# Performance work log

Measured on AMD Instinct MI355X. Metric: run time of the kernel, lower is better.

## Reference

```python
import jax, jax.numpy as jnp
import numpy as np
from jax import lax

H = 145; W = 145; BANDS = 200; D_MODEL = 128; NUM_CLASSES = 17
# Mamba2 defaults: expand=2, headdim=64, d_state=128, d_conv=4, ngroups=1
D_INNER = 256; NHEADS = 4; HEADDIM = 64; D_STATE = 128; D_CONV = 4
D_IN_PROJ = 2 * D_INNER + 2 * D_STATE + NHEADS  # 772
CONV_DIM = D_INNER + 2 * D_STATE                # 512


def _gelu(x):
    return jax.nn.gelu(x, approximate=False)


def _ln(x, g, b, eps=1e-5):
    m = jnp.mean(x, -1, keepdims=True)
    v = jnp.mean((x - m) ** 2, -1, keepdims=True)
    return (x - m) * lax.rsqrt(v + eps) * g + b


def _adaptive_pool_last(x, out):
    # PyTorch AdaptiveAvgPool semantics along the last axis via integral image
    L = x.shape[-1]
    i = np.arange(out)
    starts = (i * L) // out
    ends = -((-(i + 1) * L) // out)  # ceil((i+1)*L/out)
    cs = jnp.concatenate([jnp.zeros(x.shape[:-1] + (1,), x.dtype), jnp.cumsum(x, -1)], -1)
    return (cs[..., ends] - cs[..., starts]) / jnp.asarray(ends - starts, x.dtype)


def _mamba2(u, in_w, conv_w, conv_b, dt_bias, A_log, D, norm_w, out_w):
    # u: (L, D_MODEL). Faithful Mamba2 reference path (batch=1 squeezed).
    L = u.shape[0]
    zxbcdt = u @ in_w                      # (L, 772)
    z = zxbcdt[:, :D_INNER]                # (L, 256)
    xBC = zxbcdt[:, D_INNER:2 * D_INNER + 2 * D_STATE]  # (L, 512)
    dt = jax.nn.softplus(zxbcdt[:, -NHEADS:] + dt_bias)  # (L, 4)
    # causal depthwise conv1d, kernel D_CONV, then SiLU
    xp = jnp.pad(xBC, ((D_CONV - 1, 0), (0, 0)))
    xBC = sum(xp[k:k + L] * conv_w[:, k] for k in range(D_CONV)) + conv_b
    xBC = jax.nn.silu(xBC)
    xh = xBC[:, :D_INNER].reshape(L, NHEADS, HEADDIM)     # (L, h, p)
    Bm = xBC[:, D_INNER:D_INNER + D_STATE]                # (L, n)
    Cm = xBC[:, D_INNER + D_STATE:]                       # (L, n)
    A = -jnp.exp(A_log)                                   # (h,)

    def step(state, inp):
        dt_t, x_t, B_t, C_t = inp          # (h,), (h,p), (n,), (n,)
        dA = jnp.exp(dt_t * A)             # (h,)
        state = state * dA[:, None, None] + (dt_t[:, None] * x_t)[:, :, None] * B_t[None, None, :]
        y_t = jnp.einsum('hpn,n->hp', state, C_t)
        return state, y_t

    s0 = jnp.zeros((NHEADS, HEADDIM, D_STATE), u.dtype)
    _, y = lax.scan(step, s0, (dt, xh, Bm, Cm))           # y: (L, h, p)
    y = y + D[None, :, None] * xh
    y = y.reshape(L, D_INNER) * jax.nn.silu(z)            # gated
    y = y * lax.rsqrt(jnp.mean(y * y, -1, keepdims=True) + 1e-5) * norm_w  # RMSNormGated
    return y @ out_w                                      # (L, D_MODEL)


def _forward(x, ln_pre_g, ln_pre_b, fe_w1, fe_b1, fe_w2, fe_b2,
             cv_w1, cv_b1, cv_w2, cv_b2, mp_w, mp_b, mp_ln_g, mp_ln_b,
             m_in_w, m_conv_w, m_conv_b, m_dt_bias, m_A_log, m_D, m_norm_w, m_out_w,
             cls_ln_g, cls_ln_b, cls_w1, cls_b1, cls_w2, cls_b2, cls_w3, cls_b3):
    h, w, _ = x.shape
    xn = _ln(x, ln_pre_g, ln_pre_b)
    # MLP feature branch
    f = _gelu(xn @ fe_w1 + fe_b1)
    f = _gelu(f @ fe_w2 + fe_b2)                          # (h, w, 128)
    # conv branch
    c = jnp.transpose(xn, (2, 0, 1))[None]                # (1, bands, h, w)
    dn = ('NCHW', 'OIHW', 'NCHW')
    c = lax.conv_general_dilated(c, cv_w1, (1, 1), [(2, 2), (2, 2)], dimension_numbers=dn)
    c = _gelu(c + cv_b1[None, :, None, None])             # (1, 32, 147, 147)
    c = lax.conv_general_dilated(c, cv_w2, (1, 1), [(1, 1), (1, 1)], dimension_numbers=dn)
    c = _gelu(c + cv_b2[None, :, None, None])             # (1, 64, 147, 147)
    c = _adaptive_pool_last(c, W)                         # pool width -> 145
    c = _adaptive_pool_last(c.swapaxes(-1, -2), H).swapaxes(-1, -2)  # pool height
    conv_feat = jnp.transpose(c[0], (1, 2, 0))            # (145, 145, 64)
    comb = jnp.concatenate([f, conv_feat], -1).reshape(h * w, 192)
    p = _gelu(_ln(comb @ mp_w + mp_b, mp_ln_g, mp_ln_b))  # (L, d_model)
    m = _mamba2(p, m_in_w, m_conv_w, m_conv_b, m_dt_bias, m_A_log, m_D, m_norm_w, m_out_w)
    r = m.reshape(h, w, D_MODEL)
    o = _ln(r, cls_ln_g, cls_ln_b)
    o = _gelu(o @ cls_w1 + cls_b1)
    o = _gelu(o @ cls_w2 + cls_b2)
    return o @ cls_w3 + cls_b3                            # (h, w, num_classes)


def setup_inputs() -> dict:
    key = jax.random.key(0)
    ks = jax.random.split(key, 16)
    def n(k, shape, s=0.02):
        return jax.random.normal(k, shape, jnp.float32) * s
    return dict(
        x=jax.random.normal(ks[0], (H, W, BANDS), jnp.float32),
        ln_pre_g=jnp.ones((BANDS,), jnp.float32), ln_pre_b=jnp.zeros((BANDS,), jnp.float32),
        fe_w1=n(ks[1], (BANDS, 256)), fe_b1=jnp.zeros((256,), jnp.float32),
        fe_w2=n(ks[2], (256, 128)), fe_b2=jnp.zeros((128,), jnp.float32),
        cv_w1=n(ks[3], (32, BANDS, 3, 3)), cv_b1=jnp.zeros((32,), jnp.float32),
        cv_w2=n(ks[4], (64, 32, 3, 3)), cv_b2=jnp.zeros((64,), jnp.float32),
        mp_w=n(ks[5], (192, D_MODEL)), mp_b=jnp.zeros((D_MODEL,), jnp.float32),
        mp_ln_g=jnp.ones((D_MODEL,), jnp.float32), mp_ln_b=jnp.zeros((D_MODEL,), jnp.float32),
        m_in_w=n(ks[6], (D_MODEL, D_IN_PROJ)),
        m_conv_w=n(ks[7], (CONV_DIM, D_CONV), 0.2), m_conv_b=jnp.zeros((CONV_DIM,), jnp.float32),
        m_dt_bias=jnp.full((NHEADS,), -4.0, jnp.float32),
        m_A_log=jnp.log(jnp.linspace(1.0, 16.0, NHEADS)).astype(jnp.float32),
        m_D=jnp.ones((NHEADS,), jnp.float32),
        m_norm_w=jnp.ones((D_INNER,), jnp.float32),
        m_out_w=n(ks[8], (D_INNER, D_MODEL)),
        cls_ln_g=jnp.ones((D_MODEL,), jnp.float32), cls_ln_b=jnp.zeros((D_MODEL,), jnp.float32),
        cls_w1=n(ks[9], (D_MODEL, 128)), cls_b1=jnp.zeros((128,), jnp.float32),
        cls_w2=n(ks[10], (128, 64)), cls_b2=jnp.zeros((64,), jnp.float32),
        cls_w3=n(ks[11], (64, NUM_CLASSES)), cls_b3=jnp.zeros((NUM_CLASSES,), jnp.float32),
    )


def reference(x, ln_pre_g, ln_pre_b, fe_w1, fe_b1, fe_w2, fe_b2,
              cv_w1, cv_b1, cv_w2, cv_b2, mp_w, mp_b, mp_ln_g, mp_ln_b,
              m_in_w, m_conv_w, m_conv_b, m_dt_bias, m_A_log, m_D, m_norm_w, m_out_w,
              cls_ln_g, cls_ln_b, cls_w1, cls_b1, cls_w2, cls_b2, cls_w3, cls_b3):
    return _forward(x, ln_pre_g, ln_pre_b, fe_w1, fe_b1, fe_w2, fe_b2,
                    cv_w1, cv_b1, cv_w2, cv_b2, mp_w, mp_b, mp_ln_g, mp_ln_b,
                    m_in_w, m_conv_w, m_conv_b, m_dt_bias, m_A_log, m_D, m_norm_w, m_out_w,
                    cls_ln_g, cls_ln_b, cls_w1, cls_b1, cls_w2, cls_b2, cls_w3, cls_b3)
```

## Files before the change

kernel.cpp:

```cpp
#include <hip/hip_runtime.h>
#include <math.h>

#define HW 21025
#define Hdim 145
#define Wdim 145
#define NBANDS 200
#define CONVH 147
#define CONVHW 21609
#define QC 64
#define NCH 329
#define DTP 21056
#define SP 72

typedef __attribute__((ext_vector_type(4))) float fv4;
typedef __attribute__((ext_vector_type(8))) short short8;

#define OFF_XN   ((size_t)0)
#define OFF_F1   ((size_t)4205000)
#define OFF_COMB ((size_t)9587400)
#define OFF_P    ((size_t)13624200)
#define OFF_ZX   ((size_t)16315400)
#define OFF_XBC  ((size_t)32546700)
#define OFF_S    ((size_t)43311500)
#define OFF_DT   ((size_t)54092172)
#define OFF_CT   ((size_t)54176396)
#define OFF_W    ((size_t)54177712)

__device__ __forceinline__ float gelu_f(float x){
    return 0.5f * x * (1.0f + erff(x * 0.70710678118654752440f));
}
__device__ __forceinline__ float silu_f(float x){
    return x / (1.0f + expf(-x));
}

__device__ __forceinline__ void bf16_split(float x, unsigned short& hs, unsigned short& ls){
    unsigned u = __float_as_uint(x);
    hs = (unsigned short)(u >> 16);
    float hif = __uint_as_float(u & 0xFFFF0000u);
    float lof = x - hif;
    ls = (unsigned short)(__float_as_uint(lof) >> 16);
}
__device__ __forceinline__ unsigned pack2(unsigned short a, unsigned short b){
    return (unsigned)a | ((unsigned)b << 16);
}

template<int ACT>
__global__ void ln_kernel(const float* __restrict__ in, const float* __restrict__ g,
                          const float* __restrict__ b, float* __restrict__ out, int D){
    int row = blockIdx.x, tid = threadIdx.x;
    const float* r = in + (size_t)row * D;
    float s = 0.f, s2 = 0.f;
    for (int i = tid; i < D; i += 256){ float v = r[i]; s += v; s2 += v*v; }
    __shared__ float r1[4], r2[4];
    #pragma unroll
    for (int o = 32; o > 0; o >>= 1){ s += __shfl_down(s, o); s2 += __shfl_down(s2, o); }
    if ((tid & 63) == 0){ r1[tid >> 6] = s; r2[tid >> 6] = s2; }
    __syncthreads();
    float S = r1[0] + r1[1] + r1[2] + r1[3];
    float S2 = r2[0] + r2[1] + r2[2] + r2[3];
    float mean = S / (float)D;
    float var = S2 / (float)D - mean * mean;
    float rs = rsqrtf(fmaxf(var, 0.f) + 1e-5f);
    float* o_ = out + (size_t)row * D;
    for (int i = tid; i < D; i += 256){
        float v = (r[i] - mean) * rs * g[i] + b[i];
        if (ACT == 1) v = gelu_f(v);
        o_[i] = v;
    }
}

template<int ACT>
__global__ __launch_bounds__(256) void gemm_mfma(const float* __restrict__ A, int lda,
                                                 const float* __restrict__ B,
                                                 const float* __restrict__ bias,
                                                 float* __restrict__ C, int ldc,
                                                 int M, int N, int K){
    const int SA = 40;
    __shared__ __align__(16) unsigned short Ah[128 * SA], Al[128 * SA];
    __shared__ __align__(16) unsigned short Bh[64 * SA],  Bl[64 * SA];
    int tid = threadIdx.x;
    int lane = tid & 63, wid = tid >> 6;
    int wy = wid >> 1, wx = wid & 1;
    int bm = blockIdx.y * 128, bn = blockIdx.x * 64;
    int l15 = lane & 15, g = lane >> 4;

    fv4 acc[4][2];
    #pragma unroll
    for (int i = 0; i < 4; i++)
        #pragma unroll
        for (int j = 0; j < 2; j++) acc[i][j] = (fv4){0.f,0.f,0.f,0.f};

    int am = tid >> 1;
    int aq = (tid & 1) * 4;
    bool arow_ok = (bm + am) < M;
    int bn_t = tid & 63;
    int bk8 = (tid >> 6) * 8;
    bool bcol_ok = (bn + bn_t) < N;

    int nK = (K + 31) / 32;
    for (int ks = 0; ks < nK; ks++){
        int k0 = ks * 32;
        const float* Ap = A + (size_t)(bm + am) * lda + k0;
        #pragma unroll
        for (int f = 0; f < 4; f++){
            int kq = aq + f;
            fv4 v = (fv4){0.f,0.f,0.f,0.f};
            if (arow_ok && (k0 + kq * 4 + 4) <= K)
                v = *reinterpret_cast<const fv4*>(Ap + kq * 4);
            unsigned short hs[4], ls[4];
            #pragma unroll
            for (int j = 0; j < 4; j++) bf16_split(v[j], hs[j], ls[j]);
            unsigned off = am * SA + kq * 4;
            *reinterpret_cast<uint2*>(&Ah[off]) = make_uint2(pack2(hs[0],hs[1]), pack2(hs[2],hs[3]));
            *reinterpret_cast<uint2*>(&Al[off]) = make_uint2(pack2(ls[0],ls[1]), pack2(ls[2],ls[3]));
        }
        {
            unsigned short hs[8], ls[8];
            #pragma unroll
            for (int j = 0; j < 8; j++){
                int kk = k0 + bk8 + j;
                float v = (bcol_ok && kk < K) ? B[(size_t)kk * N + bn + bn_t] : 0.f;
                bf16_split(v, hs[j], ls[j]);
            }
            unsigned off = bn_t * SA + bk8;
            *reinterpret_cast<uint4*>(&Bh[off]) = make_uint4(pack2(hs[0],hs[1]), pack2(hs[2],hs[3]),
                                                             pack2(hs[4],hs[5]), pack2(hs[6],hs[7]));
            *reinterpret_cast<uint4*>(&Bl[off]) = make_uint4(pack2(ls[0],ls[1]), pack2(ls[2],ls[3]),
                                                             pack2(ls[4],ls[5]), pack2(ls[6],ls[7]));
        }
        __syncthreads();
        short8 afh[4], afl[4], bfh[2], bfl[2];
        #pragma unroll
        for (int mi = 0; mi < 4; mi++){
            unsigned off = (wy * 64 + mi * 16 + l15) * SA + g * 8;
            afh[mi] = *reinterpret_cast<const short8*>(&Ah[off]);
            afl[mi] = *reinterpret_cast<const short8*>(&Al[off]);
        }
        #pragma unroll
        for (int ni = 0; ni < 2; ni++){
            unsigned off = (wx * 32 + ni * 16 + l15) * SA + g * 8;
            bfh[ni] = *reinterpret_cast<const short8*>(&Bh[off]);
            bfl[ni] = *reinterpret_cast<const short8*>(&Bl[off]);
        }
        #pragma unroll
        for (int mi = 0; mi < 4; mi++)
            #pragma unroll
            for (int ni = 0; ni < 2; ni++){
                acc[mi][ni] = __builtin_amdgcn_mfma_f32_16x16x32_bf16(afh[mi], bfh[ni], acc[mi][ni], 0, 0, 0);
                acc[mi][ni] = __builtin_amdgcn_mfma_f32_16x16x32_bf16(afh[mi], bfl[ni], acc[mi][ni], 0, 0, 0);
                acc[mi][ni] = __builtin_amdgcn_mfma_f32_16x16x32_bf16(afl[mi], bfh[ni], acc[mi][ni], 0, 0, 0);
            }
        __syncthreads();
    }
    #pragma unroll
    for (int mi = 0; mi < 4; mi++){
        #pragma unroll
        for (int ni = 0; ni < 2; ni++){
            int cc = bn + wx * 32 + ni * 16 + l15;
            if (cc >= N) continue;
            float bv = bias ? bias[cc] : 0.f;
            #pragma unroll
            for (int j = 0; j < 4; j++){
                int rr = bm + wy * 64 + mi * 16 + g * 4 + j;
                if (rr >= M) continue;
                float v = acc[mi][ni][j] + bv;
                if (ACT == 1) v = gelu_f(v);
                C[(size_t)rr * ldc + cc] = v;
            }
        }
    }
}

template<int IC, int OC, int NCHUNK>
__global__ void prep_w(const float* __restrict__ w, unsigned short* __restrict__ Wh,
                       unsigned short* __restrict__ Wl){
    const int KP = NCHUNK * 288;
    int idx = blockIdx.x * 256 + threadIdx.x;
    if (idx >= OC * KP) return;
    int o = idx / KP, k = idx % KP;
    int ch = k / 288, rest = k % 288, t = rest / 32, c = rest & 31;
    int ci = ch * 32 + c;
    float v = (ci < IC) ? w[((size_t)o * IC + ci) * 9 + t] : 0.f;
    unsigned short hs, ls;
    bf16_split(v, hs, ls);
    Wh[idx] = hs; Wl[idx] = ls;
}

template<int IC, int OC, int PAD, int NCHUNK, int NFRAG>
__global__ __launch_bounds__(256) void conv_mfma(const float* __restrict__ in,
                                                 int inH, int inW,
                                                 const unsigned short* __restrict__ Wh,
                                                 const unsigned short* __restrict__ Wl,
                                                 const float* __restrict__ bias,
                                                 float* __restrict__ out){
    const int KP = NCHUNK * 288;
    const int CST = 40;
    __shared__ __align__(16) unsigned short Xh[3 * 68 * CST], Xl[3 * 68 * CST];
    int y = blockIdx.y;
    int x0 = blockIdx.x * 64;
    int tid = threadIdx.x;
    int lane = tid & 63, wid = tid >> 6;
    int wy = wid >> 1, wx = wid & 1;
    int l15 = lane & 15, g = lane >> 4;

    fv4 acc[2][NFRAG];
    #pragma unroll
    for (int mi = 0; mi < 2; mi++)
        #pragma unroll
        for (int ni = 0; ni < NFRAG; ni++) acc[mi][ni] = (fv4){0.f,0.f,0.f,0.f};

    for (int ch = 0; ch < NCHUNK; ch++){
        int ci0 = ch * 32;
        if (ch > 0) __syncthreads();
        for (int e = tid; e < 3 * 68 * 8; e += 256){
            int qd = e & 7;
            int c  = (e >> 3) % 68;
            int r  = e / 544;
            int iy = y - PAD + r, ix = x0 - PAD + c;
            fv4 v = (fv4){0.f,0.f,0.f,0.f};
            if ((unsigned)iy < (unsigned)inH && (unsigned)ix < (unsigned)inW &&
                (ci0 + qd * 4 + 4) <= IC)
                v = *reinterpret_cast<const fv4*>(in + ((size_t)iy * inW + ix) * IC + ci0 + qd * 4);
            unsigned short hs[4], ls[4];
            #pragma unroll
            for (int j = 0; j < 4; j++) bf16_split(v[j], hs[j], ls[j]);
            unsigned off = (r * 68 + c) * CST + qd * 4;
            *reinterpret_cast<uint2*>(&Xh[off]) = make_uint2(pack2(hs[0],hs[1]), pack2(hs[2],hs[3]));
            *reinterpret_cast<uint2*>(&Xl[off]) = make_uint2(pack2(ls[0],ls[1]), pack2(ls[2],ls[3]));
        }
        __syncthreads();
        #pragma unroll
        for (int t = 0; t < 9; t++){
            int ky = t / 3, kx = t % 3;
            short8 ah[2], al[2], bh[NFRAG], bl[NFRAG];
            #pragma unroll
            for (int mi = 0; mi < 2; mi++){
                unsigned off = (ky * 68 + wy * 32 + mi * 16 + l15 + kx) * CST + g * 8;
                ah[mi] = *reinterpret_cast<const short8*>(&Xh[off]);
                al[mi] = *reinterpret_cast<const short8*>(&Xl[off]);
            }
            #pragma unroll
            for (int ni = 0; ni < NFRAG; ni++){
                int oc = wx * (16 * NFRAG) + ni * 16 + l15;
                size_t woff = (size_t)oc * KP + ch * 288 + t * 32 + g * 8;
                bh[ni] = *reinterpret_cast<const short8*>(&Wh[woff]);
                bl[ni] = *reinterpret_cast<const short8*>(&Wl[woff]);
            }
            #pragma unroll
            for (int mi = 0; mi < 2; mi++)
                #pragma unroll
                for (int ni = 0; ni < NFRAG; ni++){
                    acc[mi][ni] = __builtin_amdgcn_mfma_f32_16x16x32_bf16(ah[mi], bh[ni], acc[mi][ni], 0, 0, 0);
                    acc[mi][ni] = __builtin_amdgcn_mfma_f32_16x16x32_bf16(ah[mi], bl[ni], acc[mi][ni], 0, 0, 0);
                    acc[mi][ni] = __builtin_amdgcn_mfma_f32_16x16x32_bf16(al[mi], bh[ni], acc[mi][ni], 0, 0, 0);
                }
        }
    }
    #pragma unroll
    for (int mi = 0; mi < 2; mi++)
        #pragma unroll
        for (int ni = 0; ni < NFRAG; ni++){
            int oc = wx * (16 * NFRAG) + ni * 16 + l15;
            float bv = bias[oc];
            #pragma unroll
            for (int j = 0; j < 4; j++){
                int x = x0 + wy * 32 + mi * 16 + g * 4 + j;
                if (x >= CONVH) continue;
                out[((size_t)y * CONVH + x) * OC + oc] = gelu_f(acc[mi][ni][j] + bv);
            }
        }
}

__global__ void pool_kernel(const float* __restrict__ c2, float* __restrict__ comb){
    int idx = blockIdx.x * 256 + threadIdx.x;
    if (idx >= HW * 64) return;
    int o = idx & 63;
    int pix = idx >> 6;
    int xo = pix % Wdim, yo = pix / Wdim;
    int ys = yo * CONVH / Hdim, ye = ((yo + 1) * CONVH + Hdim - 1) / Hdim;
    int xs = xo * CONVH / Wdim, xe = ((xo + 1) * CONVH + Wdim - 1) / Wdim;
    float s = 0.f;
    for (int yy = ys; yy < ye; yy++)
        for (int xx = xs; xx < xe; xx++)
            s += c2[((size_t)yy * CONVH + xx) * 64 + o];
    comb[(size_t)pix * 192 + 128 + o] = s / (float)((ye - ys) * (xe - xs));
}

__global__ void dt_kernel(const float* __restrict__ zx, const float* __restrict__ dt_bias,
                          float* __restrict__ dtbT){
    int t = blockIdx.x * 256 + threadIdx.x;
    int h = blockIdx.y;
    if (t >= HW) return;
    float v = zx[(size_t)t * 772 + 768 + h] + dt_bias[h];
    dtbT[h * DTP + t] = (v > 20.f) ? v : log1pf(expf(v));
}

__global__ __launch_bounds__(256) void conv1d_tiled(const float* __restrict__ zx,
                                                    const float* __restrict__ w,
                                                    const float* __restrict__ b,
                                                    float* __restrict__ xbc){
    __shared__ float xs[67 * 128];
    __shared__ float wc[4 * 128];
    __shared__ float bc[128];
    int t0 = blockIdx.y * 64;
    int c0 = blockIdx.x * 128;
    int tid = threadIdx.x;
    for (int e = tid; e < 67 * 128; e += 256){
        int rr = e >> 7, cc = e & 127;
        int t = t0 - 3 + rr;
        xs[e] = (t >= 0 && t < HW) ? zx[(size_t)t * 772 + 256 + c0 + cc] : 0.f;
    }
    if (tid < 128){
        bc[tid] = b[c0 + tid];
        #pragma unroll
        for (int k = 0; k < 4; k++) wc[k * 128 + tid] = w[(c0 + tid) * 4 + k];
    }
    __syncthreads();
    for (int e = tid; e < 64 * 128; e += 256){
        int tt = e >> 7, cc = e & 127;
        if (t0 + tt >= HW) continue;
        float acc = bc[cc];
        #pragma unroll
        for (int k = 0; k < 4; k++) acc += xs[(tt + k) * 128 + cc] * wc[k * 128 + cc];
        xbc[(size_t)(t0 + tt) * 512 + c0 + cc] = silu_f(acc);
    }
}

__device__ __forceinline__ void chunk_cumsum_t(const float* __restrict__ dtbT, int t0, int Q,
                                               int h, const float* __restrict__ A_log,
                                               float* cum, float* dth){
    int tid = threadIdx.x;
    if (tid < 64){
        float d = (tid < Q) ? dtbT[h * DTP + t0 + tid] : 0.f;
        dth[tid] = d;
        float A = -expf(A_log[h]);
        float a = d * A;
        #pragma unroll
        for (int off = 1; off < 64; off <<= 1){
            float u = __shfl_up(a, off);
            if (tid >= off) a += u;
        }
        cum[tid] = a;
    }
    __syncthreads();
}

__global__ __launch_bounds__(256) void ssd_phaseA(const float* __restrict__ xbc,
                                                  const float* __restrict__ dtbT,
                                                  const float* __restrict__ A_log,
                                                  float* __restrict__ S,
                                                  float* __restrict__ chunkT){
    __shared__ __align__(16) unsigned short BTh[128 * SP], BTl[128 * SP];
    __shared__ __align__(16) unsigned short XTh[64 * SP],  XTl[64 * SP];
    __shared__ float cum[64], dth[64], wln[64];
    int bid = blockIdx.x, c = bid >> 2, h = bid & 3;
    int t0 = c * QC, Q = min(QC, HW - t0);
    int tid = threadIdx.x;
    chunk_cumsum_t(dtbT, t0, Q, h, A_log, cum, dth);
    float T = cum[Q - 1];
    if (tid == 0) chunkT[bid] = T;
    if (tid < 64) wln[tid] = (tid < Q) ? __expf(T - cum[tid]) * dth[tid] : 0.f;
    __syncthreads();
    for (int e2 = tid; e2 < 4096; e2 += 256){
        int nn = e2 & 127, sp = e2 >> 7;
        int s0 = 2 * sp;
        float v0 = (s0 < Q)     ? xbc[(size_t)(t0 + s0) * 512 + 256 + nn] : 0.f;
        float v1 = (s0 + 1 < Q) ? xbc[(size_t)(t0 + s0 + 1) * 512 + 256 + nn] : 0.f;
        unsigned short h0, l0, h1, l1;
        bf16_split(v0, h0, l0); bf16_split(v1, h1, l1);
        *reinterpret_cast<unsigned*>(&BTh[nn * SP + s0]) = pack2(h0, h1);
        *reinterpret_cast<unsigned*>(&BTl[nn * SP + s0]) = pack2(l0, l1);
    }
    for (int e2 = tid; e2 < 2048; e2 += 256){
        int pp = e2 & 63, sp = e2 >> 6;
        int s0 = 2 * sp;
        float v0 = (s0 < Q)     ? xbc[(size_t)(t0 + s0) * 512 + h * 64 + pp] * wln[s0] : 0.f;
        float v1 = (s0 + 1 < Q) ? xbc[(size_t)(t0 + s0 + 1) * 512 + h * 64 + pp] * wln[s0 + 1] : 0.f;
        unsigned short h0, l0, h1, l1;
        bf16_split(v0, h0, l0); bf16_split(v1, h1, l1);
        *reinterpret_cast<unsigned*>(&XTh[pp * SP + s0]) = pack2(h0, h1);
        *reinterpret_cast<unsigned*>(&XTl[pp * SP + s0]) = pack2(l0, l1);
    }
    __syncthreads();
    int lane = tid & 63, wid = tid >> 6;
    int wy = wid >> 1, wx = wid & 1;
    int l15 = lane & 15, g = lane >> 4;
    fv4 acc[2][4];
    #pragma unroll
    for (int mi = 0; mi < 2; mi++)
        #pragma unroll
        for (int ni = 0; ni < 4; ni++) acc[mi][ni] = (fv4){0.f,0.f,0.f,0.f};
    #pragma unroll
    for (int ks = 0; ks < 2; ks++){
        short8 ah[2], al[2], bh_[4], bl_[4];
        #pragma unroll
        for (int mi = 0; mi < 2; mi++){
            unsigned off = (wy * 32 + mi * 16 + l15) * SP + ks * 32 + g * 8;
            ah[mi] = *reinterpret_cast<const short8*>(&XTh[off]);
            al[mi] = *reinterpret_cast<const short8*>(&XTl[off]);
        }
        #pragma unroll
        for (int ni = 0; ni < 4; ni++){
            unsigned off = (wx * 64 + ni * 16 + l15) * SP + ks * 32 + g * 8;
            bh_[ni] = *reinterpret_cast<const short8*>(&BTh[off]);
            bl_[ni] = *reinterpret_cast<const short8*>(&BTl[off]);
        }
        #pragma unroll
        for (int mi = 0; mi < 2; mi++)
            #pragma unroll
            for (int ni = 0; ni < 4; ni++){
                acc[mi][ni] = __builtin_amdgcn_mfma_f32_16x16x32_bf16(ah[mi], bh_[ni], acc[mi][ni], 0, 0, 0);
                acc[mi][ni] = __builtin_amdgcn_mfma_f32_16x16x32_bf16(ah[mi], bl_[ni], acc[mi][ni], 0, 0, 0);
                acc[mi][ni] = __builtin_amdgcn_mfma_f32_16x16x32_bf16(al[mi], bh_[ni], acc[mi][ni], 0, 0, 0);
            }
    }
    size_t sb = (size_t)bid * 8192;
    #pragma unroll
    for (int mi = 0; mi < 2; mi++)
        #pragma unroll
        for (int ni = 0; ni < 4; ni++)
            #pragma unroll
            for (int j = 0; j < 4; j++){
                int p = wy * 32 + mi * 16 + g * 4 + j;
                int n = wx * 64 + ni * 16 + l15;
                S[sb + p * 128 + n] = acc[mi][ni][j];
            }
}

__global__ __launch_bounds__(256) void ssd_phaseB(float* __restrict__ S,
                                                  const float* __restrict__ chunkT){
    __shared__ float e[NCH];
    int tid = threadIdx.x;
    int idx = blockIdx.x * 256 + tid;
    int h = idx >> 13, pn = idx & 8191;
    for (int c = tid; c < NCH; c += 256) e[c] = __expf(chunkT[c * 4 + h]);
    __syncthreads();
    #define LDS_(cc) S[((size_t)((cc) * 4 + h)) * 8192 + pn]
    float b0 = LDS_(0), b1 = LDS_(1), b2 = LDS_(2), b3 = LDS_(3);
    float s = 0.f;
    int c = 0;
    for (; c + 8 <= NCH; c += 4){
        float n0 = LDS_(c + 4), n1 = LDS_(c + 5), n2 = LDS_(c + 6), n3 = LDS_(c + 7);
        LDS_(c) = s;     s = fmaf(s, e[c],     b0);
        LDS_(c + 1) = s; s = fmaf(s, e[c + 1], b1);
        LDS_(c + 2) = s; s = fmaf(s, e[c + 2], b2);
        LDS_(c + 3) = s; s = fmaf(s, e[c + 3], b3);
        b0 = n0; b1 = n1; b2 = n2; b3 = n3;
    }
    for (; c < NCH; c++){
        float nx = (c + 4 < NCH) ? LDS_(c + 4) : 0.f;
        float loc = b0; b0 = b1; b1 = b2; b2 = b3; b3 = nx;
        LDS_(c) = s;
        s = fmaf(s, e[c], loc);
    }
    #undef LDS_
}

__global__ __launch_bounds__(256) void ssd_phaseC(const float* __restrict__ xbc,
                                                  const float* __restrict__ dtbT,
                                                  const float* __restrict__ A_log,
                                                  const float* __restrict__ Dvec,
                                                  const float* __restrict__ S,
                                                  float* __restrict__ y){
    __shared__ __align__(16) unsigned short Ch_[64 * SP], Cl_[64 * SP];
    __shared__ __align__(16) unsigned short Bh_[64 * SP], Bl_[64 * SP];
    __shared__ __align__(16) unsigned short Sh_[64 * SP], Sl_[64 * SP];
    __shared__ float cum[64], dth[64];
    int bid = blockIdx.x, c = bid >> 2, h = bid & 3;
    int t0 = c * QC, Q = min(QC, HW - t0);
    int tid = threadIdx.x;
    chunk_cumsum_t(dtbT, t0, Q, h, A_log, cum, dth);
    int lane = tid & 63, wid = tid >> 6;
    int wy = wid >> 1, wx = wid & 1;
    int l15 = lane & 15, g = lane >> 4;
    size_t sb = (size_t)bid * 8192;

    fv4 accG[2][2], accA[2][2];
    #pragma unroll
    for (int mi = 0; mi < 2; mi++)
        #pragma unroll
        for (int ni = 0; ni < 2; ni++){ accG[mi][ni] = (fv4){0.f,0.f,0.f,0.f}; accA[mi][ni] = (fv4){0.f,0.f,0.f,0.f}; }

    #pragma unroll
    for (int ks = 0; ks < 2; ks++){
        int n0 = ks * 64;
        for (int e2 = tid; e2 < 2048; e2 += 256){
            int rr = e2 >> 5, n2 = (e2 & 31) * 2;
            bool ok = rr < Q;
            float c0 = ok ? xbc[(size_t)(t0 + rr) * 512 + 384 + n0 + n2]     : 0.f;
            float c1 = ok ? xbc[(size_t)(t0 + rr) * 512 + 384 + n0 + n2 + 1] : 0.f;
            float b0 = ok ? xbc[(size_t)(t0 + rr) * 512 + 256 + n0 + n2]     : 0.f;
            float b1 = ok ? xbc[(size_t)(t0 + rr) * 512 + 256 + n0 + n2 + 1] : 0.f;
            float s0 = S[sb + rr * 128 + n0 + n2];
            float s1 = S[sb + rr * 128 + n0 + n2 + 1];
            unsigned short xh0, xl0, xh1, xl1;
            bf16_split(c0, xh0, xl0); bf16_split(c1, xh1, xl1);
            *reinterpret_cast<unsigned*>(&Ch_[rr * SP + n2]) = pack2(xh0, xh1);
            *reinterpret_cast<unsigned*>(&Cl_[rr * SP + n2]) = pack2(xl0, xl1);
            bf16_split(b0, xh0, xl0); bf16_split(b1, xh1, xl1);
            *reinterpret_cast<unsigned*>(&Bh_[rr * SP + n2]) = pack2(xh0, xh1);
            *reinterpret_cast<unsigned*>(&Bl_[rr * SP + n2]) = pack2(xl0, xl1);
            bf16_split(s0, xh0, xl0); bf16_split(s1, xh1, xl1);
            *reinterpret_cast<unsigned*>(&Sh_[rr * SP + n2]) = pack2(xh0, xh1);
            *reinterpret_cast<unsigned*>(&Sl_[rr * SP + n2]) = pack2(xl0, xl1);
        }
        __syncthreads();
        #pragma unroll
        for (int kk = 0; kk < 2; kk++){
            short8 ah[2], al[2], gh[2], gl[2], sh[2], sl[2];
            #pragma unroll
            for (int mi = 0; mi < 2; mi++){
                unsigned off = (wy * 32 + mi * 16 + l15) * SP + kk * 32 + g * 8;
                ah[mi] = *reinterpret_cast<const short8*>(&Ch_[off]);
                al[mi] = *reinterpret_cast<const short8*>(&Cl_[off]);
            }
            #pragma unroll
            for (int ni = 0; ni < 2; ni++){
                unsigned off = (wx * 32 + ni * 16 + l15) * SP + kk * 32 + g * 8;
                gh[ni] = *reinterpret_cast<const short8*>(&Bh_[off]);
                gl[ni] = *reinterpret_cast<const short8*>(&Bl_[off]);
                sh[ni] = *reinterpret_cast<const short8*>(&Sh_[off]);
                sl[ni] = *reinterpret_cast<const short8*>(&Sl_[off]);
            }
            #pragma unroll
            for (int mi = 0; mi < 2; mi++)
                #pragma unroll
                for (int ni = 0; ni < 2; ni++){
                    accG[mi][ni] = __builtin_amdgcn_mfma_f32_16x16x32_bf16(ah[mi], gh[ni], accG[mi][ni], 0, 0, 0);
                    accG[mi][ni] = __builtin_amdgcn_mfma_f32_16x16x32_bf16(ah[mi], gl[ni], accG[mi][ni], 0, 0, 0);
                    accG[mi][ni] = __builtin_amdgcn_mfma_f32_16x16x32_bf16(al[mi], gh[ni], accG[mi][ni], 0, 0, 0);
                    accA[mi][ni] = __builtin_amdgcn_mfma_f32_16x16x32_bf16(ah[mi], sh[ni], accA[mi][ni], 0, 0, 0);
                    accA[mi][ni] = __builtin_amdgcn_mfma_f32_16x16x32_bf16(ah[mi], sl[ni], accA[mi][ni], 0, 0, 0);
                    accA[mi][ni] = __builtin_amdgcn_mfma_f32_16x16x32_bf16(al[mi], sh[ni], accA[mi][ni], 0, 0, 0);
                }
        }
        __syncthreads();
    }
    #pragma unroll
    for (int mi = 0; mi < 2; mi++)
        #pragma unroll
        for (int ni = 0; ni < 2; ni++)
            #pragma unroll
            for (int j = 0; j < 4; j++){
                int t = wy * 32 + mi * 16 + g * 4 + j;
                int s = wx * 32 + ni * 16 + l15;
                float pv = 0.f;
                if (s <= t && s < Q)
                    pv = accG[mi][ni][j] * __expf(cum[t] - cum[s]) * dth[s];
                unsigned short hs, ls;
                bf16_split(pv, hs, ls);
                Bh_[t * SP + s] = hs;
                Bl_[t * SP + s] = ls;
            }
    for (int e2 = tid; e2 < 2048; e2 += 256){
        int pp = e2 & 63, sp = e2 >> 6;
        int s0 = 2 * sp;
        float v0 = (s0 < Q)     ? xbc[(size_t)(t0 + s0) * 512 + h * 64 + pp] : 0.f;
        float v1 = (s0 + 1 < Q) ? xbc[(size_t)(t0 + s0 + 1) * 512 + h * 64 + pp] : 0.f;
        unsigned short h0, l0, h1, l1;
        bf16_split(v0, h0, l0); bf16_split(v1, h1, l1);
        *reinterpret_cast<unsigned*>(&Ch_[pp * SP + s0]) = pack2(h0, h1);
        *reinterpret_cast<unsigned*>(&Cl_[pp * SP + s0]) = pack2(l0, l1);
    }
    __syncthreads();
    fv4 accY[2][2];
    #pragma unroll
    for (int mi = 0; mi < 2; mi++)
        #pragma unroll
        for (int ni = 0; ni < 2; ni++)
            #pragma unroll
            for (int j = 0; j < 4; j++){
                int t = wy * 32 + mi * 16 + g * 4 + j;
                accY[mi][ni][j] = __expf(cum[t]) * accA[mi][ni][j];
            }
    #pragma unroll
    for (int kk = 0; kk < 2; kk++){
        short8 ph[2], pl[2], xh[2], xl[2];
        #pragma unroll
        for (int mi = 0; mi < 2; mi++){
            unsigned off = (wy * 32 + mi * 16 + l15) * SP + kk * 32 + g * 8;
            ph[mi] = *reinterpret_cast<const short8*>(&Bh_[off]);
            pl[mi] = *reinterpret_cast<const short8*>(&Bl_[off]);
        }
        #pragma unroll
        for (int ni = 0; ni < 2; ni++){
            unsigned off = (wx * 32 + ni * 16 + l15) * SP + kk * 32 + g * 8;
            xh[ni] = *reinterpret_cast<const short8*>(&Ch_[off]);
            xl[ni] = *reinterpret_cast<const short8*>(&Cl_[off]);
        }
        #pragma unroll
        for (int mi = 0; mi < 2; mi++)
            #pragma unroll
            for (int ni = 0; ni < 2; ni++){
                accY[mi][ni] = __builtin_amdgcn_mfma_f32_16x16x32_bf16(ph[mi], xh[ni], accY[mi][ni], 0, 0, 0);
                accY[mi][ni] = __builtin_amdgcn_mfma_f32_16x16x32_bf16(ph[mi], xl[ni], accY[mi][ni], 0, 0, 0);
                accY[mi][ni] = __builtin_amdgcn_mfma_f32_16x16x32_bf16(pl[mi], xh[ni], accY[mi][ni], 0, 0, 0);
            }
    }
    float Dh = Dvec[h];
    #pragma unroll
    for (int mi = 0; mi < 2; mi++)
        #pragma unroll
        for (int ni = 0; ni < 2; ni++)
            #pragma unroll
            for (int j = 0; j < 4; j++){
                int t = wy * 32 + mi * 16 + g * 4 + j;
                if (t >= Q) continue;
                int p = wx * 32 + ni * 16 + l15;
                float xv = xbc[(size_t)(t0 + t) * 512 + h * 64 + p];
                y[(size_t)(t0 + t) * 256 + h * 64 + p] = accY[mi][ni][j] + Dh * xv;
            }
}

__global__ void gated_rms_kernel(float* __restrict__ y, const float* __restrict__ zx,
                                 const float* __restrict__ nw){
    int row = blockIdx.x, tid = threadIdx.x;
    float v = y[(size_t)row * 256 + tid];
    float z = zx[(size_t)row * 772 + tid];
    v *= silu_f(z);
    float s = v * v;
    __shared__ float r1[4];
    #pragma unroll
    for (int o = 32; o > 0; o >>= 1) s += __shfl_down(s, o);
    if ((tid & 63) == 0) r1[tid >> 6] = s;
    __syncthreads();
    float S = r1[0] + r1[1] + r1[2] + r1[3];
    float rs = rsqrtf(S / 256.f + 1e-5f);
    y[(size_t)row * 256 + tid] = v * rs * nw[tid];
}

extern "C" void kernel_launch(void* const* d_in, const int* in_sizes, int n_in,
                              void* d_out, int out_size, void* d_ws, size_t ws_size,
                              hipStream_t stream){
    (void)in_sizes; (void)n_in; (void)out_size; (void)ws_size;
    const float* x        = (const float*)d_in[0];
    const float* ln_pre_g = (const float*)d_in[1];
    const float* ln_pre_b = (const float*)d_in[2];
    const float* fe_w1    = (const float*)d_in[3];
    const float* fe_b1    = (const float*)d_in[4];
    const float* fe_w2    = (const float*)d_in[5];
    const float* fe_b2    = (const float*)d_in[6];
    const float* cv_w1    = (const float*)d_in[7];
    const float* cv_b1    = (const float*)d_in[8];
    const float* cv_w2    = (const float*)d_in[9];
    const float* cv_b2    = (const float*)d_in[10];
    const float* mp_w     = (const float*)d_in[11];
    const float* mp_b     = (const float*)d_in[12];
    const float* mp_ln_g  = (const float*)d_in[13];
    const float* mp_ln_b  = (const float*)d_in[14];
    const float* m_in_w   = (const float*)d_in[15];
    const float* m_conv_w = (const float*)d_in[16];
    const float* m_conv_b = (const float*)d_in[17];
    const float* m_dtb    = (const float*)d_in[18];
    const float* m_A_log  = (const float*)d_in[19];
    const float* m_D      = (const float*)d_in[20];
    const float* m_norm_w = (const float*)d_in[21];
    const float* m_out_w  = (const float*)d_in[22];
    const float* cls_ln_g = (const float*)d_in[23];
    const float* cls_ln_b = (const float*)d_in[24];
    const float* cls_w1   = (const float*)d_in[25];
    const float* cls_b1   = (const float*)d_in[26];
    const float* cls_w2   = (const float*)d_in[27];
    const float* cls_b2   = (const float*)d_in[28];
    const float* cls_w3   = (const float*)d_in[29];
    const float* cls_b3   = (const float*)d_in[30];

    float* ws   = (float*)d_ws;
    float* xn   = ws + OFF_XN;
    float* f1   = ws + OFF_F1;
    float* comb = ws + OFF_COMB;
    float* p    = ws + OFF_P;
    float* zx   = ws + OFF_ZX;
    float* xbc  = ws + OFF_XBC;
    float* Sbuf = ws + OFF_S;
    float* dtbT = ws + OFF_DT;
    float* chkT = ws + OFF_CT;
    float* c1h  = ws + OFF_XBC;
    float* c2h  = ws + OFF_XBC + 691488;
    float* pr   = ws + OFF_XN;
    float* ybuf = ws + OFF_F1;
    float* mo   = ws + OFF_COMB;
    float* cls0 = ws + OFF_XN;
    float* cls1 = ws + OFF_P;
    float* cls2 = ws + OFF_COMB + 2691200;
    unsigned short* W1h = (unsigned short*)(ws + OFF_W);
    unsigned short* W1l = (unsigned short*)(ws + OFF_W + 32256);
    unsigned short* W2h = (unsigned short*)(ws + OFF_W + 64512);
    unsigned short* W2l = (unsigned short*)(ws + OFF_W + 73728);

    prep_w<200, 32, 7><<<(32 * 2016 + 255) / 256, 256, 0, stream>>>(cv_w1, W1h, W1l);
    prep_w<32, 64, 1><<<(64 * 288 + 255) / 256, 256, 0, stream>>>(cv_w2, W2h, W2l);
    ln_kernel<0><<<HW, 256, 0, stream>>>(x, ln_pre_g, ln_pre_b, xn, NBANDS);
    gemm_mfma<1><<<dim3(4, 165), 256, 0, stream>>>(xn, 200, fe_w1, fe_b1, f1, 256, HW, 256, 200);
    gemm_mfma<1><<<dim3(2, 165), 256, 0, stream>>>(f1, 256, fe_w2, fe_b2, comb, 192, HW, 128, 256);
    conv_mfma<200, 32, 2, 7, 1><<<dim3(3, CONVH), 256, 0, stream>>>(xn, Hdim, Wdim, W1h, W1l, cv_b1, c1h);
    conv_mfma<32, 64, 1, 1, 2><<<dim3(3, CONVH), 256, 0, stream>>>(c1h, CONVH, CONVH, W2h, W2l, cv_b2, c2h);
    pool_kernel<<<(HW * 64 + 255) / 256, 256, 0, stream>>>(c2h, comb);
    gemm_mfma<0><<<dim3(2, 165), 256, 0, stream>>>(comb, 192, mp_w, mp_b, pr, 128, HW, 128, 192);
    ln_kernel<1><<<HW, 256, 0, stream>>>(pr, mp_ln_g, mp_ln_b, p, 128);
    gemm_mfma<0><<<dim3(13, 165), 256, 0, stream>>>(p, 128, m_in_w, (const float*)nullptr, zx, 772, HW, 772, 128);
    dt_kernel<<<dim3((HW + 255) / 256, 4), 256, 0, stream>>>(zx, m_dtb, dtbT);
    conv1d_tiled<<<dim3(4, NCH), 256, 0, stream>>>(zx, m_conv_w, m_conv_b, xbc);
    ssd_phaseA<<<NCH * 4, 256, 0, stream>>>(xbc, dtbT, m_A_log, Sbuf, chkT);
    ssd_phaseB<<<128, 256, 0, stream>>>(Sbuf, chkT);
    ssd_phaseC<<<NCH * 4, 256, 0, stream>>>(xbc, dtbT, m_A_log, m_D, Sbuf, ybuf);
    gated_rms_kernel<<<HW, 256, 0, stream>>>(ybuf, zx, m_norm_w);
    gemm_mfma<0><<<dim3(2, 165), 256, 0, stream>>>(ybuf, 256, m_out_w, (const float*)nullptr, mo, 128, HW, 128, 256);
    ln_kernel<0><<<HW, 256, 0, stream>>>(mo, cls_ln_g, cls_ln_b, cls0, 128);
    gemm_mfma<1><<<dim3(2, 165), 256, 0, stream>>>(cls0, 128, cls_w1, cls_b1, cls1, 128, HW, 128, 128);
    gemm_mfma<1><<<dim3(1, 165), 256, 0, stream>>>(cls1, 128, cls_w2, cls_b2, cls2, 64, HW, 64, 128);
    gemm_mfma<0><<<dim3(1, 165), 256, 0, stream>>>(cls2, 64, cls_w3, cls_b3, (float*)d_out, 17, HW, 17, 64);
}
```

Before: 517.6 us.

## Store SSD chunk states pre-split as packed bf16 pairs and load phaseC operands directly

Chunk states S are now written as packed hi/lo bf16 pairs in one 32-bit word, so phaseC can unpack them straight into MFMA operands. PhaseC's first stage also skips the LDS staging of C, B and S: each lane loads its fragment from global memory with vector loads and splits it in registers. Both changes target LDS traffic, barriers and repeated split work. Block IDs are also remapped so the 8 chunks sharing a head land on neighbouring blocks, which should help L2 locality. In exchange phaseB pays a pack and unpack per element, the state is carried at split-bf16 precision, and the grid is padded so some blocks exit early.

```diff
diff --git a/kernel.cpp b/kernel.cpp
--- a/kernel.cpp
+++ b/kernel.cpp
@@ -11,6 +11,7 @@
 #define NCH 329
 #define DTP 21056
 #define SP 72
+#define SSD_GRID 1344
 
 typedef __attribute__((ext_vector_type(4))) float fv4;
 typedef __attribute__((ext_vector_type(8))) short short8;
@@ -42,6 +43,38 @@
 }
 __device__ __forceinline__ unsigned pack2(unsigned short a, unsigned short b){
     return (unsigned)a | ((unsigned)b << 16);
+}
+__device__ __forceinline__ unsigned packsplit(float x){
+    unsigned short hs, ls;
+    bf16_split(x, hs, ls);
+    return ((unsigned)hs << 16) | (unsigned)ls;
+}
+__device__ __forceinline__ float unpackf(unsigned u){
+    return __uint_as_float(u & 0xFFFF0000u) + __uint_as_float(u << 16);
+}
+__device__ __forceinline__ void split8g(const float* p, short8& h8, short8& l8){
+    fv4 v0 = *reinterpret_cast<const fv4*>(p);
+    fv4 v1 = *reinterpret_cast<const fv4*>(p + 4);
+    unsigned short hs, ls;
+    #pragma unroll
+    for (int j = 0; j < 4; j++){
+        bf16_split(v0[j], hs, ls); h8[j] = (short)hs; l8[j] = (short)ls;
+        bf16_split(v1[j], hs, ls); h8[4 + j] = (short)hs; l8[4 + j] = (short)ls;
+    }
+}
+__device__ __forceinline__ void unpack8(const unsigned* p, short8& h8, short8& l8){
+    uint4 a = *reinterpret_cast<const uint4*>(p);
+    uint4 b = *reinterpret_cast<const uint4*>(p + 4);
+    unsigned v0 = a.x, v1 = a.y, v2 = a.z, v3 = a.w;
+    unsigned v4 = b.x, v5 = b.y, v6 = b.z, v7 = b.w;
+    h8[0]=(short)(v0>>16); l8[0]=(short)(v0&0xFFFFu);
+    h8[1]=(short)(v1>>16); l8[1]=(short)(v1&0xFFFFu);
+    h8[2]=(short)(v2>>16); l8[2]=(short)(v2&0xFFFFu);
+    h8[3]=(short)(v3>>16); l8[3]=(short)(v3&0xFFFFu);
+    h8[4]=(short)(v4>>16); l8[4]=(short)(v4&0xFFFFu);
+    h8[5]=(short)(v5>>16); l8[5]=(short)(v5&0xFFFFu);
+    h8[6]=(short)(v6>>16); l8[6]=(short)(v6&0xFFFFu);
+    h8[7]=(short)(v7>>16); l8[7]=(short)(v7&0xFFFFu);
 }
 
 template<int ACT>
@@ -345,20 +378,28 @@
     __syncthreads();
 }
 
+__device__ __forceinline__ bool ssd_decode(int bid, int& c, int& h){
+    int m = bid & 7, rest = bid >> 3;
+    h = rest & 3;
+    c = (rest >> 2) * 8 + m;
+    return c < NCH;
+}
+
 __global__ __launch_bounds__(256) void ssd_phaseA(const float* __restrict__ xbc,
                                                   const float* __restrict__ dtbT,
                                                   const float* __restrict__ A_log,
-                                                  float* __restrict__ S,
+                                                  unsigned* __restrict__ Sp,
                                                   float* __restrict__ chunkT){
     __shared__ __align__(16) unsigned short BTh[128 * SP], BTl[128 * SP];
     __shared__ __align__(16) unsigned short XTh[64 * SP],  XTl[64 * SP];
     __shared__ float cum[64], dth[64], wln[64];
-    int bid = blockIdx.x, c = bid >> 2, h = bid & 3;
+    int c, h;
+    if (!ssd_decode(blockIdx.x, c, h)) return;
     int t0 = c * QC, Q = min(QC, HW - t0);
     int tid = threadIdx.x;
     chunk_cumsum_t(dtbT, t0, Q, h, A_log, cum, dth);
     float T = cum[Q - 1];
-    if (tid == 0) chunkT[bid] = T;
+    if (tid == 0) chunkT[c * 4 + h] = T;
     if (tid < 64) wln[tid] = (tid < Q) ? __expf(T - cum[tid]) * dth[tid] : 0.f;
     __syncthreads();
     for (int e2 = tid; e2 < 4096; e2 += 256){
@@ -414,7 +455,7 @@
                 acc[mi][ni] = __builtin_amdgcn_mfma_f32_16x16x32_bf16(al[mi], bh_[ni], acc[mi][ni], 0, 0, 0);
             }
     }
-    size_t sb = (size_t)bid * 8192;
+    size_t sb = (size_t)(c * 4 + h) * 8192;
     #pragma unroll
     for (int mi = 0; mi < 2; mi++)
         #pragma unroll
@@ -423,11 +464,11 @@
             for (int j = 0; j < 4; j++){
                 int p = wy * 32 + mi * 16 + g * 4 + j;
                 int n = wx * 64 + ni * 16 + l15;
-                S[sb + p * 128 + n] = acc[mi][ni][j];
-            }
-}
-
-__global__ __launch_bounds__(256) void ssd_phaseB(float* __restrict__ S,
+                Sp[sb + p * 128 + n] = packsplit(acc[mi][ni][j]);
+            }
+}
+
+__global__ __launch_bounds__(256) void ssd_phaseB(unsigned* __restrict__ Sp,
                                                   const float* __restrict__ chunkT){
     __shared__ float e[NCH];
     int tid = threadIdx.x;
@@ -435,45 +476,52 @@
     int h = idx >> 13, pn = idx & 8191;
     for (int c = tid; c < NCH; c += 256) e[c] = __expf(chunkT[c * 4 + h]);
     __syncthreads();
-    #define LDS_(cc) S[((size_t)((cc) * 4 + h)) * 8192 + pn]
-    float b0 = LDS_(0), b1 = LDS_(1), b2 = LDS_(2), b3 = LDS_(3);
+    #define ADDR_(cc) Sp[((size_t)((cc) * 4 + h)) * 8192 + pn]
+    unsigned r0 = ADDR_(0), r1 = ADDR_(1), r2 = ADDR_(2), r3 = ADDR_(3);
     float s = 0.f;
     int c = 0;
     for (; c + 8 <= NCH; c += 4){
-        float n0 = LDS_(c + 4), n1 = LDS_(c + 5), n2 = LDS_(c + 6), n3 = LDS_(c + 7);
-        LDS_(c) = s;     s = fmaf(s, e[c],     b0);
-        LDS_(c + 1) = s; s = fmaf(s, e[c + 1], b1);
-        LDS_(c + 2) = s; s = fmaf(s, e[c + 2], b2);
-        LDS_(c + 3) = s; s = fmaf(s, e[c + 3], b3);
-        b0 = n0; b1 = n1; b2 = n2; b3 = n3;
+        unsigned n0 = ADDR_(c + 4), n1 = ADDR_(c + 5), n2 = ADDR_(c + 6), n3 = ADDR_(c + 7);
+        ADDR_(c) = packsplit(s);     s = fmaf(s, e[c],     unpackf(r0));
+        ADDR_(c + 1) = packsplit(s); s = fmaf(s, e[c + 1], unpackf(r1));
+        ADDR_(c + 2) = packsplit(s); s = fmaf(s, e[c + 2], unpackf(r2));
+        ADDR_(c + 3) = packsplit(s); s = fmaf(s, e[c + 3], unpackf(r3));
+        r0 = n0; r1 = n1; r2 = n2; r3 = n3;
     }
     for (; c < NCH; c++){
-        float nx = (c + 4 < NCH) ? LDS_(c + 4) : 0.f;
-        float loc = b0; b0 = b1; b1 = b2; b2 = b3; b3 = nx;
-        LDS_(c) = s;
+        unsigned nx = (c + 4 < NCH) ? ADDR_(c + 4) : 0u;
+        float loc = unpackf(r0); r0 = r1; r1 = r2; r2 = r3; r3 = nx;
+        ADDR_(c) = packsplit(s);
         s = fmaf(s, e[c], loc);
     }
-    #undef LDS_
+    #undef ADDR_
 }
 
 __global__ __launch_bounds__(256) void ssd_phaseC(const float* __restrict__ xbc,
                                                   const float* __restrict__ dtbT,
                                                   const float* __restrict__ A_log,
                                                   const float* __restrict__ Dvec,
-                                                  const float* __restrict__ S,
+                                                  const unsigned* __restrict__ Sp,
                                                   float* __restrict__ y){
-    __shared__ __align__(16) unsigned short Ch_[64 * SP], Cl_[64 * SP];
-    __shared__ __align__(16) unsigned short Bh_[64 * SP], Bl_[64 * SP];
-    __shared__ __align__(16) unsigned short Sh_[64 * SP], Sl_[64 * SP];
+    __shared__ __align__(16) unsigned short U0h[64 * SP], U0l[64 * SP];
+    __shared__ __align__(16) unsigned short U1h[64 * SP], U1l[64 * SP];
     __shared__ float cum[64], dth[64];
-    int bid = blockIdx.x, c = bid >> 2, h = bid & 3;
+    int c, h;
+    if (!ssd_decode(blockIdx.x, c, h)) return;
     int t0 = c * QC, Q = min(QC, HW - t0);
     int tid = threadIdx.x;
     chunk_cumsum_t(dtbT, t0, Q, h, A_log, cum, dth);
     int lane = tid & 63, wid = tid >> 6;
     int wy = wid >> 1, wx = wid & 1;
     int l15 = lane & 15, g = lane >> 4;
-    size_t sb = (size_t)bid * 8192;
+
+    int trow[2], srow[2], prow[2];
+    #pragma unroll
+    for (int i = 0; i < 2; i++){
+        trow[i] = min(t0 + wy * 32 + i * 16 + l15, HW - 1);
+        srow[i] = min(t0 + wx * 32 + i * 16 + l15, HW - 1);
+        prow[i] = wx * 32 + i * 16 + l15;
+    }
 
     fv4 accG[2][2], accA[2][2];
     #pragma unroll
@@ -481,60 +529,29 @@
         #pragma unroll
         for (int ni = 0; ni < 2; ni++){ accG[mi][ni] = (fv4){0.f,0.f,0.f,0.f}; accA[mi][ni] = (fv4){0.f,0.f,0.f,0.f}; }
 
-    #pragma unroll
-    for (int ks = 0; ks < 2; ks++){
-        int n0 = ks * 64;
-        for (int e2 = tid; e2 < 2048; e2 += 256){
-            int rr = e2 >> 5, n2 = (e2 & 31) * 2;
-            bool ok = rr < Q;
-            float c0 = ok ? xbc[(size_t)(t0 + rr) * 512 + 384 + n0 + n2]     : 0.f;
-            float c1 = ok ? xbc[(size_t)(t0 + rr) * 512 + 384 + n0 + n2 + 1] : 0.f;
-            float b0 = ok ? xbc[(size_t)(t0 + rr) * 512 + 256 + n0 + n2]     : 0.f;
-            float b1 = ok ? xbc[(size_t)(t0 + rr) * 512 + 256 + n0 + n2 + 1] : 0.f;
-            float s0 = S[sb + rr * 128 + n0 + n2];
-            float s1 = S[sb + rr * 128 + n0 + n2 + 1];
-            unsigned short xh0, xl0, xh1, xl1;
-            bf16_split(c0, xh0, xl0); bf16_split(c1, xh1, xl1);
-            *reinterpret_cast<unsigned*>(&Ch_[rr * SP + n2]) = pack2(xh0, xh1);
-            *reinterpret_cast<unsigned*>(&Cl_[rr * SP + n2]) = pack2(xl0, xl1);
-            bf16_split(b0, xh0, xl0); bf16_split(b1, xh1, xl1);
-            *reinterpret_cast<unsigned*>(&Bh_[rr * SP + n2]) = pack2(xh0, xh1);
-            *reinterpret_cast<unsigned*>(&Bl_[rr * SP + n2]) = pack2(xl0, xl1);
-            bf16_split(s0, xh0, xl0); bf16_split(s1, xh1, xl1);
-            *reinterpret_cast<unsigned*>(&Sh_[rr * SP + n2]) = pack2(xh0, xh1);
-            *reinterpret_cast<unsigned*>(&Sl_[rr * SP + n2]) = pack2(xl0, xl1);
-        }
-        __syncthreads();
-        #pragma unroll
-        for (int kk = 0; kk < 2; kk++){
-            short8 ah[2], al[2], gh[2], gl[2], sh[2], sl[2];
-            #pragma unroll
-            for (int mi = 0; mi < 2; mi++){
-                unsigned off = (wy * 32 + mi * 16 + l15) * SP + kk * 32 + g * 8;
-                ah[mi] = *reinterpret_cast<const short8*>(&Ch_[off]);
-                al[mi] = *reinterpret_cast<const short8*>(&Cl_[off]);
-            }
+    const unsigned* Sbase = Sp + (size_t)(c * 4 + h) * 8192;
+    #pragma unroll
+    for (int k0 = 0; k0 < 128; k0 += 32){
+        short8 ah[2], al[2], bh[2], bl[2], sh[2], sl[2];
+        #pragma unroll
+        for (int mi = 0; mi < 2; mi++)
+            split8g(xbc + (size_t)trow[mi] * 512 + 384 + k0 + g * 8, ah[mi], al[mi]);
+        #pragma unroll
+        for (int ni = 0; ni < 2; ni++){
+            split8g(xbc + (size_t)srow[ni] * 512 + 256 + k0 + g * 8, bh[ni], bl[ni]);
+            unpack8(Sbase + prow[ni] * 128 + k0 + g * 8, sh[ni], sl[ni]);
+        }
+        #pragma unroll
+        for (int mi = 0; mi < 2; mi++)
             #pragma unroll
             for (int ni = 0; ni < 2; ni++){
-                unsigned off = (wx * 32 + ni * 16 + l15) * SP + kk * 32 + g * 8;
-                gh[ni] = *reinterpret_cast<const short8*>(&Bh_[off]);
-                gl[ni] = *reinterpret_cast<const short8*>(&Bl_[off]);
-                sh[ni] = *reinterpret_cast<const short8*>(&Sh_[off]);
-                sl[ni] = *reinterpret_cast<const short8*>(&Sl_[off]);
-            }
-            #pragma unroll
-            for (int mi = 0; mi < 2; mi++)
-                #pragma unroll
-                for (int ni = 0; ni < 2; ni++){
-                    accG[mi][ni] = __builtin_amdgcn_mfma_f32_16x16x32_bf16(ah[mi], gh[ni], accG[mi][ni], 0, 0, 0);
-                    accG[mi][ni] = __builtin_amdgcn_mfma_f32_16x16x32_bf16(ah[mi], gl[ni], accG[mi][ni], 0, 0, 0);
-                    accG[mi][ni] = __builtin_amdgcn_mfma_f32_16x16x32_bf16(al[mi], gh[ni], accG[mi][ni], 0, 0, 0);
-                    accA[mi][ni] = __builtin_amdgcn_mfma_f32_16x16x32_bf16(ah[mi], sh[ni], accA[mi][ni], 0, 0, 0);
-                    accA[mi][ni] = __builtin_amdgcn_mfma_f32_16x16x32_bf16(ah[mi], sl[ni], accA[mi][ni], 0, 0, 0);
-                    accA[mi][ni] = __builtin_amdgcn_mfma_f32_16x16x32_bf16(al[mi], sh[ni], accA[mi][ni], 0, 0, 0);
-                }
-        }
-        __syncthreads();
+                accG[mi][ni] = __builtin_amdgcn_mfma_f32_16x16x32_bf16(ah[mi], bh[ni], accG[mi][ni], 0, 0, 0);
+                accG[mi][ni] = __builtin_amdgcn_mfma_f32_16x16x32_bf16(ah[mi], bl[ni], accG[mi][ni], 0, 0, 0);
+                accG[mi][ni] = __builtin_amdgcn_mfma_f32_16x16x32_bf16(al[mi], bh[ni], accG[mi][ni], 0, 0, 0);
+                accA[mi][ni] = __builtin_amdgcn_mfma_f32_16x16x32_bf16(ah[mi], sh[ni], accA[mi][ni], 0, 0, 0);
+                accA[mi][ni] = __builtin_amdgcn_mfma_f32_16x16x32_bf16(ah[mi], sl[ni], accA[mi][ni], 0, 0, 0);
+                accA[mi][ni] = __builtin_amdgcn_mfma_f32_16x16x32_bf16(al[mi], sh[ni], accA[mi][ni], 0, 0, 0);
+            }
     }
     #pragma unroll
     for (int mi = 0; mi < 2; mi++)
@@ -549,8 +566,8 @@
                     pv = accG[mi][ni][j] * __expf(cum[t] - cum[s]) * dth[s];
                 unsigned short hs, ls;
                 bf16_split(pv, hs, ls);
-                Bh_[t * SP + s] = hs;
-                Bl_[t * SP + s] = ls;
+                U0h[t * SP + s] = hs;
+                U0l[t * SP + s] = ls;
             }
     for (int e2 = tid; e2 < 2048; e2 += 256){
         int pp = e2 & 63, sp = e2 >> 6;
@@ -559,8 +576,8 @@
         float v1 = (s0 + 1 < Q) ? xbc[(size_t)(t0 + s0 + 1) * 512 + h * 64 + pp] : 0.f;
         unsigned short h0, l0, h1, l1;
         bf16_split(v0, h0, l0); bf16_split(v1, h1, l1);
-        *reinterpret_cast<unsigned*>(&Ch_[pp * SP + s0]) = pack2(h0, h1);
-        *reinterpret_cast<unsigned*>(&Cl_[pp * SP + s0]) = pack2(l0, l1);
+        *reinterpret_cast<unsigned*>(&U1h[pp * SP + s0]) = pack2(h0, h1);
+        *reinterpret_cast<unsigned*>(&U1l[pp * SP + s0]) = pack2(l0, l1);
     }
     __syncthreads();
     fv4 accY[2][2];
@@ -579,14 +596,14 @@
         #pragma unroll
         for (int mi = 0; mi < 2; mi++){
             unsigned off = (wy * 32 + mi * 16 + l15) * SP + kk * 32 + g * 8;
-            ph[mi] = *reinterpret_cast<const short8*>(&Bh_[off]);
-            pl[mi] = *reinterpret_cast<const short8*>(&Bl_[off]);
+            ph[mi] = *reinterpret_cast<const short8*>(&U0h[off]);
+            pl[mi] = *reinterpret_cast<const short8*>(&U0l[off]);
         }
         #pragma unroll
         for (int ni = 0; ni < 2; ni++){
             unsigned off = (wx * 32 + ni * 16 + l15) * SP + kk * 32 + g * 8;
-            xh[ni] = *reinterpret_cast<const short8*>(&Ch_[off]);
-            xl[ni] = *reinterpret_cast<const short8*>(&Cl_[off]);
+            xh[ni] = *reinterpret_cast<const short8*>(&U1h[off]);
+            xl[ni] = *reinterpret_cast<const short8*>(&U1l[off]);
         }
         #pragma unroll
         for (int mi = 0; mi < 2; mi++)
@@ -672,7 +689,7 @@
     float* p    = ws + OFF_P;
     float* zx   = ws + OFF_ZX;
     float* xbc  = ws + OFF_XBC;
-    float* Sbuf = ws + OFF_S;
+    unsigned* Sp = (unsigned*)(ws + OFF_S);
     float* dtbT = ws + OFF_DT;
     float* chkT = ws + OFF_CT;
     float* c1h  = ws + OFF_XBC;
@@ -701,9 +718,9 @@
     gemm_mfma<0><<<dim3(13, 165), 256, 0, stream>>>(p, 128, m_in_w, (const float*)nullptr, zx, 772, HW, 772, 128);
     dt_kernel<<<dim3((HW + 255) / 256, 4), 256, 0, stream>>>(zx, m_dtb, dtbT);
     conv1d_tiled<<<dim3(4, NCH), 256, 0, stream>>>(zx, m_conv_w, m_conv_b, xbc);
-    ssd_phaseA<<<NCH * 4, 256, 0, stream>>>(xbc, dtbT, m_A_log, Sbuf, chkT);
-    ssd_phaseB<<<128, 256, 0, stream>>>(Sbuf, chkT);
-    ssd_phaseC<<<NCH * 4, 256, 0, stream>>>(xbc, dtbT, m_A_log, m_D, Sbuf, ybuf);
+    ssd_phaseA<<<SSD_GRID, 256, 0, stream>>>(xbc, dtbT, m_A_log, Sp, chkT);
+    ssd_phaseB<<<128, 256, 0, stream>>>(Sp, chkT);
+    ssd_phaseC<<<SSD_GRID, 256, 0, stream>>>(xbc, dtbT, m_A_log, m_D, Sp, ybuf);
     gated_rms_kernel<<<HW, 256, 0, stream>>>(ybuf, zx, m_norm_w);
     gemm_mfma<0><<<dim3(2, 165), 256, 0, stream>>>(ybuf, 256, m_out_w, (const float*)nullptr, mo, 128, HW, 128, 256);
     ln_kernel<0><<<HW, 256, 0, stream>>>(mo, cls_ln_g, cls_ln_b, cls0, 128);
```

Result: no change. 518.5 us (+0.2%).
